# Kernel optimization log

Measured on AMD Instinct MI355X. Metric: run time of the kernel, lower is better.

Reference implementation:

```python
import jax, jax.numpy as jnp
import numpy as np

N_NODES = 30000
N_EDGES = 480000
N_GRAPHS = 128
D_IN = 128
D_H = 256
N_CLASSES = 60


def gcn_conv(x, src, dst, norm, W, b, num_nodes):
    # x: [N, d_in]; W: [d_out, d_in]; b: [d_out]
    h = x @ W.T                                   # [N, d_out]
    msg = h[src] * norm[:, None]                  # [E+N, d_out] gather + scale
    out = jax.ops.segment_sum(msg, dst, num_segments=num_nodes)  # scatter-add
    return out + b


def setup_inputs() -> dict:
    key = jax.random.key(0)
    ks = jax.random.split(key, 10)
    glorot = lambda k, o, i: jax.random.normal(k, (o, i), jnp.float32) * (2.0 / (o + i)) ** 0.5
    x = jax.random.normal(ks[0], (N_NODES, D_IN), jnp.float32)
    edge_index = jax.random.randint(ks[1], (2, N_EDGES), 0, N_NODES, jnp.int64)
    batch = jnp.sort(jax.random.randint(ks[2], (N_NODES,), 0, N_GRAPHS, jnp.int64))
    return {
        "x": x,
        "edge_index": edge_index,
        "batch": batch,
        "W1": glorot(ks[3], D_H, D_IN), "b1": jnp.zeros((D_H,), jnp.float32),
        "W2": glorot(ks[4], D_H, D_H),  "b2": jnp.zeros((D_H,), jnp.float32),
        "W3": glorot(ks[5], D_H, D_H),  "b3": jnp.zeros((D_H,), jnp.float32),
        "Wfc": glorot(ks[6], N_CLASSES, D_H),
        "bfc": jnp.zeros((N_CLASSES,), jnp.float32),
    }


def reference(x, edge_index, batch, W1, b1, W2, b2, W3, b3, Wfc, bfc):
    num_nodes = x.shape[0]
    # GCNConv default: add self-loops, symmetric normalization D^-1/2 A D^-1/2
    loops = jnp.arange(num_nodes, dtype=edge_index.dtype)
    src = jnp.concatenate([edge_index[0], loops])
    dst = jnp.concatenate([edge_index[1], loops])
    deg = jax.ops.segment_sum(jnp.ones_like(dst, dtype=x.dtype), dst,
                              num_segments=num_nodes)
    dinv = jnp.where(deg > 0, jax.lax.rsqrt(deg), 0.0)
    norm = dinv[src] * dinv[dst]                  # per-edge normalization

    h = jax.nn.relu(gcn_conv(x, src, dst, norm, W1, b1, num_nodes))
    h = jax.nn.relu(gcn_conv(h, src, dst, norm, W2, b2, num_nodes))
    h = jax.nn.relu(gcn_conv(h, src, dst, norm, W3, b3, num_nodes))

    # global_mean_pool over graph ids
    sums = jax.ops.segment_sum(h, batch, num_segments=N_GRAPHS)
    cnts = jax.ops.segment_sum(jnp.ones((num_nodes,), h.dtype), batch,
                               num_segments=N_GRAPHS)
    pooled = sums / jnp.maximum(cnts, 1.0)[:, None]   # [G, 256]
    return pooled @ Wfc.T + bfc                       # [G, num_classes]
```

## Files before the change

### kernel.cpp

```cpp
#include <hip/hip_runtime.h>
#include <hip/hip_bf16.h>
#include <cstdint>
#include <cstddef>
#include <type_traits>

#define NN 30000
#define NE 480000
#define NG 128
#define DIN 128
#define DH 256
#define NC 60
#define NB 118

typedef _Float16 f16x8 __attribute__((ext_vector_type(8)));
typedef _Float16 half4_t __attribute__((ext_vector_type(4)));
typedef _Float16 half2_t __attribute__((ext_vector_type(2)));
typedef float f32x4 __attribute__((ext_vector_type(4)));

__global__ __launch_bounds__(256) void k_pre(const int* __restrict__ dst, int* __restrict__ icnt,
                     const float* __restrict__ x, _Float16* __restrict__ xh,
                     const float* __restrict__ W1, const float* __restrict__ W2,
                     const float* __restrict__ W3, _Float16* __restrict__ w1h,
                     _Float16* __restrict__ w2h, _Float16* __restrict__ w3h) {
    int i = blockIdx.x * 256 + threadIdx.x;
    if (i < NE) atomicAdd(&icnt[dst[i]], 1);
    if (i < NN * DIN / 4) {
        float4 v = ((const float4*)x)[i];
        half4_t o;
        o[0] = (_Float16)v.x; o[1] = (_Float16)v.y;
        o[2] = (_Float16)v.z; o[3] = (_Float16)v.w;
        ((half4_t*)xh)[i] = o;
    }
    if (i < DH * DIN) w1h[i] = (_Float16)W1[i];
    if (i < DH * DH) {
        w2h[i] = (_Float16)W2[i];
        w3h[i] = (_Float16)W3[i];
    }
}

__global__ __launch_bounds__(256) void k_scan1(const int* __restrict__ icnt, int* __restrict__ psum,
                                               float* __restrict__ dinv) {
    __shared__ int ws[4];
    int i = blockIdx.x * 256 + threadIdx.x;
    int lane = threadIdx.x & 63, wv = threadIdx.x >> 6;
    int v = (i < NN) ? icnt[i] : 0;
    if (i < NN) dinv[i] = rsqrtf((float)(v + 1));
    #pragma unroll
    for (int off = 32; off > 0; off >>= 1) v += __shfl_down(v, off, 64);
    if (lane == 0) ws[wv] = v;
    __syncthreads();
    if (threadIdx.x == 0) psum[blockIdx.x] = ws[0] + ws[1] + ws[2] + ws[3];
}

__global__ __launch_bounds__(64) void k_scan2(const int* __restrict__ psum, int* __restrict__ poff) {
    int lane = threadIdx.x;
    int carry = 0;
    for (int base = 0; base < NB; base += 64) {
        int i = base + lane;
        int v = (i < NB) ? psum[i] : 0;
        int s = v;
        #pragma unroll
        for (int off = 1; off < 64; off <<= 1) {
            int n = __shfl_up(s, off, 64);
            if (lane >= off) s += n;
        }
        if (i < NB) poff[i] = carry + s - v;
        carry += __shfl(s, 63, 64);
    }
}

__global__ __launch_bounds__(256) void k_scan3(const int* __restrict__ icnt, const int* __restrict__ poff,
                                               int* __restrict__ row_ptr) {
    __shared__ int ws[4];
    int i = blockIdx.x * 256 + threadIdx.x;
    int lane = threadIdx.x & 63, wv = threadIdx.x >> 6;
    int v = (i < NN) ? icnt[i] : 0;
    int s = v;
    #pragma unroll
    for (int off = 1; off < 64; off <<= 1) {
        int n = __shfl_up(s, off, 64);
        if (lane >= off) s += n;
    }
    if (lane == 63) ws[wv] = s;
    __syncthreads();
    int add = 0;
    for (int j = 0; j < wv; j++) add += ws[j];
    if (i < NN) row_ptr[i] = poff[blockIdx.x] + add + s - v;
    if (blockIdx.x == 0 && threadIdx.x == 0) row_ptr[NN] = NE;
}

__global__ void k_fill(const int* __restrict__ ei, const float* __restrict__ dinv,
                       const int* __restrict__ row_ptr, int* __restrict__ cursor,
                       int* __restrict__ csr_src, float* __restrict__ csr_w) {
    int e = blockIdx.x * blockDim.x + threadIdx.x;
    if (e >= NE) return;
    int s = ei[e];
    int d = ei[NE + e];
    int pos = row_ptr[d] + atomicAdd(&cursor[d], 1);
    csr_src[pos] = s;
    csr_w[pos] = dinv[s] * dinv[d];
}

template<int D>
__global__ __launch_bounds__(256) void k_agg(const _Float16* __restrict__ tin,
                      _Float16* __restrict__ tout,
                      const int* __restrict__ row_ptr, const int* __restrict__ csr_src,
                      const float* __restrict__ csr_w, const float* __restrict__ dinv) {
    constexpr int V = D / 64;
    using vec_t = std::conditional_t<V == 4, half4_t, half2_t>;
    int node = blockIdx.x * 4 + (threadIdx.x >> 6);
    int lane = threadIdx.x & 63;
    const _Float16* base = tin + lane * V;
    float acc[V];
    #pragma unroll
    for (int u = 0; u < V; u++) acc[u] = 0.f;
    int beg = row_ptr[node], end = row_ptr[node + 1];
    int e = beg;
    for (; e + 16 <= end; e += 16) {
        int s[16]; float w[16];
        #pragma unroll
        for (int j = 0; j < 16; j++) { s[j] = csr_src[e + j]; w[j] = csr_w[e + j]; }
        vec_t r[16];
        #pragma unroll
        for (int j = 0; j < 16; j++) r[j] = *(const vec_t*)(base + (size_t)s[j] * D);
        #pragma unroll
        for (int j = 0; j < 16; j++)
            #pragma unroll
            for (int u = 0; u < V; u++) acc[u] = fmaf(w[j], (float)r[j][u], acc[u]);
    }
    for (; e + 8 <= end; e += 8) {
        int s[8]; float w[8];
        #pragma unroll
        for (int j = 0; j < 8; j++) { s[j] = csr_src[e + j]; w[j] = csr_w[e + j]; }
        vec_t r[8];
        #pragma unroll
        for (int j = 0; j < 8; j++) r[j] = *(const vec_t*)(base + (size_t)s[j] * D);
        #pragma unroll
        for (int j = 0; j < 8; j++)
            #pragma unroll
            for (int u = 0; u < V; u++) acc[u] = fmaf(w[j], (float)r[j][u], acc[u]);
    }
    for (; e < end; e++) {
        int s0 = csr_src[e];
        float w0 = csr_w[e];
        vec_t r0 = *(const vec_t*)(base + (size_t)s0 * D);
        #pragma unroll
        for (int u = 0; u < V; u++) acc[u] = fmaf(w0, (float)r0[u], acc[u]);
    }
    float dv = dinv[node];
    float sw = dv * dv;
    vec_t rv = *(const vec_t*)(base + (size_t)node * D);
    #pragma unroll
    for (int u = 0; u < V; u++) acc[u] = fmaf(sw, (float)rv[u], acc[u]);
    vec_t o;
    #pragma unroll
    for (int u = 0; u < V; u++) o[u] = (_Float16)acc[u];
    *(vec_t*)(tout + (size_t)node * D + lane * V) = o;
}

template<int K>
__global__ __launch_bounds__(256) void k_gemm(const _Float16* __restrict__ A,
        const _Float16* __restrict__ Wh,
        const float* __restrict__ bias, _Float16* __restrict__ Cb, int M) {
    __shared__ _Float16 lsA[128 * 40];
    __shared__ _Float16 lsB[128 * 40];
    int t = threadIdx.x;
    int bm = blockIdx.x * 128;
    int bn = blockIdx.y * 128;
    int lane = t & 63, wv = t >> 6;
    int wm = (wv & 1) * 64;
    int wn = (wv >> 1) * 64;
    int lm = lane & 15, q = lane >> 4;
    int r4 = t >> 2;
    int c4 = t & 3;
    int ra0 = bm + r4;       if (ra0 >= M) ra0 = M - 1;
    int ra1 = bm + 64 + r4;  if (ra1 >= M) ra1 = M - 1;
    int rb0 = bn + r4;
    int rb1 = bn + 64 + r4;

    f32x4 acc[4][4];
    #pragma unroll
    for (int i = 0; i < 4; i++)
        #pragma unroll
        for (int j = 0; j < 4; j++) acc[i][j] = (f32x4){0.f, 0.f, 0.f, 0.f};

    for (int k0 = 0; k0 < K; k0 += 32) {
        size_t ko = (size_t)k0 + c4 * 8;
        uint4 a0 = *(const uint4*)(A + (size_t)ra0 * K + ko);
        uint4 a1 = *(const uint4*)(A + (size_t)ra1 * K + ko);
        uint4 b0 = *(const uint4*)(Wh + (size_t)rb0 * K + ko);
        uint4 b1 = *(const uint4*)(Wh + (size_t)rb1 * K + ko);
        __syncthreads();
        *(uint4*)&lsA[r4 * 40 + c4 * 8] = a0;
        *(uint4*)&lsA[(64 + r4) * 40 + c4 * 8] = a1;
        *(uint4*)&lsB[r4 * 40 + c4 * 8] = b0;
        *(uint4*)&lsB[(64 + r4) * 40 + c4 * 8] = b1;
        __syncthreads();
        f16x8 bf[4];
        #pragma unroll
        for (int nt = 0; nt < 4; nt++) {
            bf[nt] = *(const f16x8*)&lsB[(wn + nt * 16 + lm) * 40 + q * 8];
        }
        #pragma unroll
        for (int mt = 0; mt < 4; mt++) {
            f16x8 af = *(const f16x8*)&lsA[(wm + mt * 16 + lm) * 40 + q * 8];
            #pragma unroll
            for (int nt = 0; nt < 4; nt++) {
                acc[mt][nt] = __builtin_amdgcn_mfma_f32_16x16x32_f16(af, bf[nt], acc[mt][nt], 0, 0, 0);
            }
        }
    }
    #pragma unroll
    for (int mt = 0; mt < 4; mt++) {
        #pragma unroll
        for (int nt = 0; nt < 4; nt++) {
            int col = bn + wn + nt * 16 + lm;
            float bv = bias[col];
            #pragma unroll
            for (int r = 0; r < 4; r++) {
                int row = bm + wm + mt * 16 + q * 4 + r;
                if (row < M) {
                    float v = fmaxf(acc[mt][nt][r] + bv, 0.f);
                    Cb[(size_t)row * 256 + col] = (_Float16)v;
                }
            }
        }
    }
}

__global__ __launch_bounds__(256) void k_pool(const _Float16* __restrict__ h, const int* __restrict__ batch,
                       float* __restrict__ sums) {
    int f = threadIdx.x;
    int r0 = blockIdx.x * 64;
    int r1 = min(r0 + 64, NN);
    float acc = 0.f;
    int cur = batch[r0];
    for (int r = r0; r < r1; r++) {
        int g = batch[r];
        if (g != cur) {
            atomicAdd(&sums[cur * DH + f], acc);
            acc = 0.f;
            cur = g;
        }
        acc += (float)h[(size_t)r * DH + f];
    }
    atomicAdd(&sums[cur * DH + f], acc);
}

__global__ __launch_bounds__(64) void k_fc(const float* __restrict__ sums, const int* __restrict__ batch,
                    const float* __restrict__ Wfc, const float* __restrict__ bfc,
                    float* __restrict__ out) {
    __shared__ float p[DH];
    int g = blockIdx.x;
    int t = threadIdx.x;
    int lo = 0, hi = NN;
    while (lo < hi) { int mid = (lo + hi) >> 1; if (batch[mid] < g) lo = mid + 1; else hi = mid; }
    int start = lo;
    hi = NN;
    while (lo < hi) { int mid = (lo + hi) >> 1; if (batch[mid] < g + 1) lo = mid + 1; else hi = mid; }
    int cnt = lo - start;
    float inv = (cnt > 0) ? 1.f / (float)cnt : 0.f;
    for (int i = t; i < DH; i += 64) p[i] = sums[g * DH + i] * inv;
    __syncthreads();
    if (t < NC) {
        float a = bfc[t];
        for (int k = 0; k < DH; k++) a = fmaf(p[k], Wfc[t * DH + k], a);
        out[g * NC + t] = a;
    }
}

extern "C" void kernel_launch(void* const* d_in, const int* in_sizes, int n_in,
                              void* d_out, int out_size, void* d_ws, size_t ws_size,
                              hipStream_t stream) {
    const float* x     = (const float*)d_in[0];
    const int*   ei    = (const int*)d_in[1];
    const int*   batch = (const int*)d_in[2];
    const float* W1 = (const float*)d_in[3];
    const float* b1 = (const float*)d_in[4];
    const float* W2 = (const float*)d_in[5];
    const float* b2 = (const float*)d_in[6];
    const float* W3 = (const float*)d_in[7];
    const float* b3 = (const float*)d_in[8];
    const float* Wfc = (const float*)d_in[9];
    const float* bfc = (const float*)d_in[10];
    float* out = (float*)d_out;

    char* wp = (char*)d_ws;
    auto alloc = [&](size_t bytes) {
        char* p = wp;
        wp += (bytes + 511) & ~(size_t)511;
        return (void*)p;
    };
    int*   icnt    = (int*)alloc((size_t)NN * 4);
    int*   row_ptr = (int*)alloc((size_t)(NN + 1) * 4);
    int*   cursor  = (int*)alloc((size_t)NN * 4);
    int*   psum    = (int*)alloc((size_t)NB * 4);
    int*   poff    = (int*)alloc((size_t)NB * 4);
    int*   csr_src = (int*)alloc((size_t)NE * 4);
    float* csr_w   = (float*)alloc((size_t)NE * 4);
    float* dinv    = (float*)alloc((size_t)NN * 4);
    _Float16* xh   = (_Float16*)alloc((size_t)NN * DIN * 2);
    _Float16* tb   = (_Float16*)alloc((size_t)NN * DH * 2);
    _Float16* hb   = (_Float16*)alloc((size_t)NN * DH * 2);
    _Float16* w1h = (_Float16*)alloc((size_t)DH * DIN * 2);
    _Float16* w2h = (_Float16*)alloc((size_t)DH * DH * 2);
    _Float16* w3h = (_Float16*)alloc((size_t)DH * DH * 2);
    float* sums    = (float*)alloc((size_t)NG * DH * 4);

    hipMemsetAsync(icnt, 0, (size_t)NN * 4, stream);
    hipMemsetAsync(cursor, 0, (size_t)NN * 4, stream);
    hipMemsetAsync(sums, 0, (size_t)NG * DH * 4, stream);

    k_pre<<<(NN * DIN / 4 + 255) / 256, 256, 0, stream>>>(ei + NE, icnt, x, xh,
                                                          W1, W2, W3, w1h, w2h, w3h);
    k_scan1<<<NB, 256, 0, stream>>>(icnt, psum, dinv);
    k_scan2<<<1, 64, 0, stream>>>(psum, poff);
    k_scan3<<<NB, 256, 0, stream>>>(icnt, poff, row_ptr);
    k_fill<<<(NE + 255) / 256, 256, 0, stream>>>(ei, dinv, row_ptr, cursor, csr_src, csr_w);

    dim3 gemm_grid((NN + 127) / 128, 2);

    k_agg<128><<<NN / 4, 256, 0, stream>>>(xh, tb, row_ptr, csr_src, csr_w, dinv);
    k_gemm<128><<<gemm_grid, 256, 0, stream>>>(tb, w1h, b1, hb, NN);
    k_agg<256><<<NN / 4, 256, 0, stream>>>(hb, tb, row_ptr, csr_src, csr_w, dinv);
    k_gemm<256><<<gemm_grid, 256, 0, stream>>>(tb, w2h, b2, hb, NN);
    k_agg<256><<<NN / 4, 256, 0, stream>>>(hb, tb, row_ptr, csr_src, csr_w, dinv);
    k_gemm<256><<<gemm_grid, 256, 0, stream>>>(tb, w3h, b3, hb, NN);

    k_pool<<<(NN + 63) / 64, 256, 0, stream>>>(hb, batch, sums);
    k_fc<<<NG, 64, 0, stream>>>(sums, batch, Wfc, bfc, out);
}
```

Measured before the change: 320.5 us.

## Fuse aggregation and GEMM per layer, merge scan passes and memsets

Each GCN layer's sparse aggregation and dense GEMM are fused into one kernel. A block aggregates 64 nodes into shared memory, then runs MFMA against W, which is read directly from global memory, and applies bias and ReLU. This removes the round trip of the intermediate aggregated tensor through global memory and halves the layer kernel launches. The scan2 kernel is folded into scan3, where each block sums the preceding partial sums itself, and the three memsets become one contiguous memset. The trade-off is lower aggregation parallelism, since each wave now handles 16 nodes serially. W is also no longer staged through LDS, so each block re-reads it from global or cache.

Measured after the change: 396.0 us. 23.6% more time.

```diff
diff --git a/kernel.cpp b/kernel.cpp
--- a/kernel.cpp
+++ b/kernel.cpp
@@ -52,27 +52,19 @@
     if (threadIdx.x == 0) psum[blockIdx.x] = ws[0] + ws[1] + ws[2] + ws[3];
 }
 
-__global__ __launch_bounds__(64) void k_scan2(const int* __restrict__ psum, int* __restrict__ poff) {
-    int lane = threadIdx.x;
-    int carry = 0;
-    for (int base = 0; base < NB; base += 64) {
-        int i = base + lane;
-        int v = (i < NB) ? psum[i] : 0;
-        int s = v;
-        #pragma unroll
-        for (int off = 1; off < 64; off <<= 1) {
-            int n = __shfl_up(s, off, 64);
-            if (lane >= off) s += n;
-        }
-        if (i < NB) poff[i] = carry + s - v;
-        carry += __shfl(s, 63, 64);
-    }
-}
-
-__global__ __launch_bounds__(256) void k_scan3(const int* __restrict__ icnt, const int* __restrict__ poff,
+__global__ __launch_bounds__(256) void k_scan3(const int* __restrict__ icnt, const int* __restrict__ psum,
                                                int* __restrict__ row_ptr) {
     __shared__ int ws[4];
-    int i = blockIdx.x * 256 + threadIdx.x;
+    __shared__ int poff_s;
+    int b = blockIdx.x;
+    if (threadIdx.x < 64) {
+        int val = 0;
+        for (int j = threadIdx.x; j < b; j += 64) val += psum[j];
+        #pragma unroll
+        for (int off = 32; off > 0; off >>= 1) val += __shfl_down(val, off, 64);
+        if (threadIdx.x == 0) poff_s = val;
+    }
+    int i = b * 256 + threadIdx.x;
     int lane = threadIdx.x & 63, wv = threadIdx.x >> 6;
     int v = (i < NN) ? icnt[i] : 0;
     int s = v;
@@ -85,8 +77,8 @@
     __syncthreads();
     int add = 0;
     for (int j = 0; j < wv; j++) add += ws[j];
-    if (i < NN) row_ptr[i] = poff[blockIdx.x] + add + s - v;
-    if (blockIdx.x == 0 && threadIdx.x == 0) row_ptr[NN] = NE;
+    if (i < NN) row_ptr[i] = poff_s + add + s - v;
+    if (b == 0 && threadIdx.x == 0) row_ptr[NN] = NE;
 }
 
 __global__ void k_fill(const int* __restrict__ ei, const float* __restrict__ dinv,
@@ -101,127 +93,107 @@
     csr_w[pos] = dinv[s] * dinv[d];
 }
 
-template<int D>
-__global__ __launch_bounds__(256) void k_agg(const _Float16* __restrict__ tin,
-                      _Float16* __restrict__ tout,
-                      const int* __restrict__ row_ptr, const int* __restrict__ csr_src,
-                      const float* __restrict__ csr_w, const float* __restrict__ dinv) {
-    constexpr int V = D / 64;
+template<int K>
+__global__ __launch_bounds__(256, 4) void k_layer(const _Float16* __restrict__ hin,
+        const _Float16* __restrict__ W, const float* __restrict__ bias,
+        _Float16* __restrict__ hout,
+        const int* __restrict__ row_ptr, const int* __restrict__ csr_src,
+        const float* __restrict__ csr_w, const float* __restrict__ dinv) {
+    constexpr int V = K / 64;
+    constexpr int LS = K + 4;
     using vec_t = std::conditional_t<V == 4, half4_t, half2_t>;
-    int node = blockIdx.x * 4 + (threadIdx.x >> 6);
-    int lane = threadIdx.x & 63;
-    const _Float16* base = tin + lane * V;
-    float acc[V];
-    #pragma unroll
-    for (int u = 0; u < V; u++) acc[u] = 0.f;
-    int beg = row_ptr[node], end = row_ptr[node + 1];
-    int e = beg;
-    for (; e + 16 <= end; e += 16) {
-        int s[16]; float w[16];
-        #pragma unroll
-        for (int j = 0; j < 16; j++) { s[j] = csr_src[e + j]; w[j] = csr_w[e + j]; }
-        vec_t r[16];
-        #pragma unroll
-        for (int j = 0; j < 16; j++) r[j] = *(const vec_t*)(base + (size_t)s[j] * D);
-        #pragma unroll
-        for (int j = 0; j < 16; j++)
+    __shared__ _Float16 lsA[64 * LS];
+    int t = threadIdx.x;
+    int lane = t & 63, wv = t >> 6;
+    int bm = blockIdx.x * 64;
+    const _Float16* gbase = hin + lane * V;
+
+    for (int i = 0; i < 16; i++) {
+        int nl = wv * 16 + i;
+        int node = bm + nl;
+        float acc[V];
+        #pragma unroll
+        for (int u = 0; u < V; u++) acc[u] = 0.f;
+        if (node < NN) {
+            int beg = row_ptr[node], end = row_ptr[node + 1];
+            int e = beg;
+            for (; e + 16 <= end; e += 16) {
+                int s[16]; float w[16];
+                #pragma unroll
+                for (int j = 0; j < 16; j++) { s[j] = csr_src[e + j]; w[j] = csr_w[e + j]; }
+                vec_t r[16];
+                #pragma unroll
+                for (int j = 0; j < 16; j++) r[j] = *(const vec_t*)(gbase + (size_t)s[j] * K);
+                #pragma unroll
+                for (int j = 0; j < 16; j++)
+                    #pragma unroll
+                    for (int u = 0; u < V; u++) acc[u] = fmaf(w[j], (float)r[j][u], acc[u]);
+            }
+            for (; e + 8 <= end; e += 8) {
+                int s[8]; float w[8];
+                #pragma unroll
+                for (int j = 0; j < 8; j++) { s[j] = csr_src[e + j]; w[j] = csr_w[e + j]; }
+                vec_t r[8];
+                #pragma unroll
+                for (int j = 0; j < 8; j++) r[j] = *(const vec_t*)(gbase + (size_t)s[j] * K);
+                #pragma unroll
+                for (int j = 0; j < 8; j++)
+                    #pragma unroll
+                    for (int u = 0; u < V; u++) acc[u] = fmaf(w[j], (float)r[j][u], acc[u]);
+            }
+            for (; e < end; e++) {
+                int s0 = csr_src[e];
+                float w0 = csr_w[e];
+                vec_t r0 = *(const vec_t*)(gbase + (size_t)s0 * K);
+                #pragma unroll
+                for (int u = 0; u < V; u++) acc[u] = fmaf(w0, (float)r0[u], acc[u]);
+            }
+            float dv = dinv[node];
+            float sw = dv * dv;
+            vec_t rv = *(const vec_t*)(gbase + (size_t)node * K);
             #pragma unroll
-            for (int u = 0; u < V; u++) acc[u] = fmaf(w[j], (float)r[j][u], acc[u]);
-    }
-    for (; e + 8 <= end; e += 8) {
-        int s[8]; float w[8];
-        #pragma unroll
-        for (int j = 0; j < 8; j++) { s[j] = csr_src[e + j]; w[j] = csr_w[e + j]; }
-        vec_t r[8];
-        #pragma unroll
-        for (int j = 0; j < 8; j++) r[j] = *(const vec_t*)(base + (size_t)s[j] * D);
-        #pragma unroll
-        for (int j = 0; j < 8; j++)
+            for (int u = 0; u < V; u++) acc[u] = fmaf(sw, (float)rv[u], acc[u]);
+        }
+        vec_t o;
+        #pragma unroll
+        for (int u = 0; u < V; u++) o[u] = (_Float16)acc[u];
+        *(vec_t*)&lsA[nl * LS + lane * V] = o;
+    }
+    __syncthreads();
+
+    int lm = lane & 15, q = lane >> 4;
+    int wn = wv * 64;
+    f32x4 acc[4][4];
+    #pragma unroll
+    for (int i = 0; i < 4; i++)
+        #pragma unroll
+        for (int j = 0; j < 4; j++) acc[i][j] = (f32x4){0.f, 0.f, 0.f, 0.f};
+    #pragma unroll
+    for (int kt = 0; kt < K / 32; kt++) {
+        f16x8 bf[4];
+        #pragma unroll
+        for (int nt = 0; nt < 4; nt++)
+            bf[nt] = *(const f16x8*)(W + (size_t)(wn + nt * 16 + lm) * K + kt * 32 + q * 8);
+        #pragma unroll
+        for (int mt = 0; mt < 4; mt++) {
+            f16x8 af = *(const f16x8*)&lsA[(mt * 16 + lm) * LS + kt * 32 + q * 8];
             #pragma unroll
-            for (int u = 0; u < V; u++) acc[u] = fmaf(w[j], (float)r[j][u], acc[u]);
-    }
-    for (; e < end; e++) {
-        int s0 = csr_src[e];
-        float w0 = csr_w[e];
-        vec_t r0 = *(const vec_t*)(base + (size_t)s0 * D);
-        #pragma unroll
-        for (int u = 0; u < V; u++) acc[u] = fmaf(w0, (float)r0[u], acc[u]);
-    }
-    float dv = dinv[node];
-    float sw = dv * dv;
-    vec_t rv = *(const vec_t*)(base + (size_t)node * D);
-    #pragma unroll
-    for (int u = 0; u < V; u++) acc[u] = fmaf(sw, (float)rv[u], acc[u]);
-    vec_t o;
-    #pragma unroll
-    for (int u = 0; u < V; u++) o[u] = (_Float16)acc[u];
-    *(vec_t*)(tout + (size_t)node * D + lane * V) = o;
-}
-
-template<int K>
-__global__ __launch_bounds__(256) void k_gemm(const _Float16* __restrict__ A,
-        const _Float16* __restrict__ Wh,
-        const float* __restrict__ bias, _Float16* __restrict__ Cb, int M) {
-    __shared__ _Float16 lsA[128 * 40];
-    __shared__ _Float16 lsB[128 * 40];
-    int t = threadIdx.x;
-    int bm = blockIdx.x * 128;
-    int bn = blockIdx.y * 128;
-    int lane = t & 63, wv = t >> 6;
-    int wm = (wv & 1) * 64;
-    int wn = (wv >> 1) * 64;
-    int lm = lane & 15, q = lane >> 4;
-    int r4 = t >> 2;
-    int c4 = t & 3;
-    int ra0 = bm + r4;       if (ra0 >= M) ra0 = M - 1;
-    int ra1 = bm + 64 + r4;  if (ra1 >= M) ra1 = M - 1;
-    int rb0 = bn + r4;
-    int rb1 = bn + 64 + r4;
-
-    f32x4 acc[4][4];
-    #pragma unroll
-    for (int i = 0; i < 4; i++)
-        #pragma unroll
-        for (int j = 0; j < 4; j++) acc[i][j] = (f32x4){0.f, 0.f, 0.f, 0.f};
-
-    for (int k0 = 0; k0 < K; k0 += 32) {
-        size_t ko = (size_t)k0 + c4 * 8;
-        uint4 a0 = *(const uint4*)(A + (size_t)ra0 * K + ko);
-        uint4 a1 = *(const uint4*)(A + (size_t)ra1 * K + ko);
-        uint4 b0 = *(const uint4*)(Wh + (size_t)rb0 * K + ko);
-        uint4 b1 = *(const uint4*)(Wh + (size_t)rb1 * K + ko);
-        __syncthreads();
-        *(uint4*)&lsA[r4 * 40 + c4 * 8] = a0;
-        *(uint4*)&lsA[(64 + r4) * 40 + c4 * 8] = a1;
-        *(uint4*)&lsB[r4 * 40 + c4 * 8] = b0;
-        *(uint4*)&lsB[(64 + r4) * 40 + c4 * 8] = b1;
-        __syncthreads();
-        f16x8 bf[4];
+            for (int nt = 0; nt < 4; nt++)
+                acc[mt][nt] = __builtin_amdgcn_mfma_f32_16x16x32_f16(af, bf[nt], acc[mt][nt], 0, 0, 0);
+        }
+    }
+    #pragma unroll
+    for (int mt = 0; mt < 4; mt++) {
         #pragma unroll
         for (int nt = 0; nt < 4; nt++) {
-            bf[nt] = *(const f16x8*)&lsB[(wn + nt * 16 + lm) * 40 + q * 8];
-        }
-        #pragma unroll
-        for (int mt = 0; mt < 4; mt++) {
-            f16x8 af = *(const f16x8*)&lsA[(wm + mt * 16 + lm) * 40 + q * 8];
-            #pragma unroll
-            for (int nt = 0; nt < 4; nt++) {
-                acc[mt][nt] = __builtin_amdgcn_mfma_f32_16x16x32_f16(af, bf[nt], acc[mt][nt], 0, 0, 0);
-            }
-        }
-    }
-    #pragma unroll
-    for (int mt = 0; mt < 4; mt++) {
-        #pragma unroll
-        for (int nt = 0; nt < 4; nt++) {
-            int col = bn + wn + nt * 16 + lm;
+            int col = wn + nt * 16 + lm;
             float bv = bias[col];
             #pragma unroll
             for (int r = 0; r < 4; r++) {
-                int row = bm + wm + mt * 16 + q * 4 + r;
-                if (row < M) {
+                int row = bm + mt * 16 + q * 4 + r;
+                if (row < NN) {
                     float v = fmaxf(acc[mt][nt][r] + bv, 0.f);
-                    Cb[(size_t)row * 256 + col] = (_Float16)v;
+                    hout[(size_t)row * 256 + col] = (_Float16)v;
                 }
             }
         }
@@ -292,41 +264,34 @@
         return (void*)p;
     };
     int*   icnt    = (int*)alloc((size_t)NN * 4);
+    int*   cursor  = (int*)alloc((size_t)NN * 4);
+    float* sums    = (float*)alloc((size_t)NG * DH * 4);
+    size_t zlen = (char*)wp - (char*)icnt;
     int*   row_ptr = (int*)alloc((size_t)(NN + 1) * 4);
-    int*   cursor  = (int*)alloc((size_t)NN * 4);
     int*   psum    = (int*)alloc((size_t)NB * 4);
-    int*   poff    = (int*)alloc((size_t)NB * 4);
     int*   csr_src = (int*)alloc((size_t)NE * 4);
     float* csr_w   = (float*)alloc((size_t)NE * 4);
     float* dinv    = (float*)alloc((size_t)NN * 4);
     _Float16* xh   = (_Float16*)alloc((size_t)NN * DIN * 2);
-    _Float16* tb   = (_Float16*)alloc((size_t)NN * DH * 2);
-    _Float16* hb   = (_Float16*)alloc((size_t)NN * DH * 2);
+    _Float16* hA   = (_Float16*)alloc((size_t)NN * DH * 2);
+    _Float16* hB   = (_Float16*)alloc((size_t)NN * DH * 2);
     _Float16* w1h = (_Float16*)alloc((size_t)DH * DIN * 2);
     _Float16* w2h = (_Float16*)alloc((size_t)DH * DH * 2);
     _Float16* w3h = (_Float16*)alloc((size_t)DH * DH * 2);
-    float* sums    = (float*)alloc((size_t)NG * DH * 4);
-
-    hipMemsetAsync(icnt, 0, (size_t)NN * 4, stream);
-    hipMemsetAsync(cursor, 0, (size_t)NN * 4, stream);
-    hipMemsetAsync(sums, 0, (size_t)NG * DH * 4, stream);
+
+    hipMemsetAsync(icnt, 0, zlen, stream);
 
     k_pre<<<(NN * DIN / 4 + 255) / 256, 256, 0, stream>>>(ei + NE, icnt, x, xh,
                                                           W1, W2, W3, w1h, w2h, w3h);
     k_scan1<<<NB, 256, 0, stream>>>(icnt, psum, dinv);
-    k_scan2<<<1, 64, 0, stream>>>(psum, poff);
-    k_scan3<<<NB, 256, 0, stream>>>(icnt, poff, row_ptr);
+    k_scan3<<<NB, 256, 0, stream>>>(icnt, psum, row_ptr);
     k_fill<<<(NE + 255) / 256, 256, 0, stream>>>(ei, dinv, row_ptr, cursor, csr_src, csr_w);
 
-    dim3 gemm_grid((NN + 127) / 128, 2);
-
-    k_agg<128><<<NN / 4, 256, 0, stream>>>(xh, tb, row_ptr, csr_src, csr_w, dinv);
-    k_gemm<128><<<gemm_grid, 256, 0, stream>>>(tb, w1h, b1, hb, NN);
-    k_agg<256><<<NN / 4, 256, 0, stream>>>(hb, tb, row_ptr, csr_src, csr_w, dinv);
-    k_gemm<256><<<gemm_grid, 256, 0, stream>>>(tb, w2h, b2, hb, NN);
-    k_agg<256><<<NN / 4, 256, 0, stream>>>(hb, tb, row_ptr, csr_src, csr_w, dinv);
-    k_gemm<256><<<gemm_grid, 256, 0, stream>>>(tb, w3h, b3, hb, NN);
-
-    k_pool<<<(NN + 63) / 64, 256, 0, stream>>>(hb, batch, sums);
+    int lgrid = (NN + 63) / 64;
+    k_layer<128><<<lgrid, 256, 0, stream>>>(xh, w1h, b1, hA, row_ptr, csr_src, csr_w, dinv);
+    k_layer<256><<<lgrid, 256, 0, stream>>>(hA, w2h, b2, hB, row_ptr, csr_src, csr_w, dinv);
+    k_layer<256><<<lgrid, 256, 0, stream>>>(hB, w3h, b3, hA, row_ptr, csr_src, csr_w, dinv);
+
+    k_pool<<<(NN + 63) / 64, 256, 0, stream>>>(hA, batch, sums);
     k_fc<<<NG, 64, 0, stream>>>(sums, batch, Wfc, bfc, out);
 }
```
